# Optimization experiments

Measured on AMD Instinct MI355X. Metric: run time of the kernel, lower is better.

The kernel has to match this reference:

```python
import jax, jax.numpy as jnp
import numpy as np

N, HID, L, NC = 2048, 256, 4, 10
D0, D1, D2 = HID, HID // 2, HID // 8   # dims for degrees l=0,1,2
H, DH = 4, HID // 4                    # heads for degree-0 attention
F = D0 + D1 + D2                       # invariant feature width
C2 = float(np.sqrt(3.0))


def setup_inputs() -> dict:
    key = jax.random.key(0)
    ks = jax.random.split(key, 16)

    def w(k, shape, fan):
        return jax.random.normal(k, shape, jnp.float32) / np.float32(np.sqrt(fan))

    return {
        "x": jax.random.uniform(ks[0], (N, 118), jnp.float32),
        "pos": jax.random.normal(ks[1], (N, 3), jnp.float32) * 3.0,
        "emb_W": w(ks[2], (118, D0), 118),
        "emb_b": jnp.zeros((D0,), jnp.float32),
        "Wq": w(ks[3], (L, F, H * DH), F),
        "Wk": w(ks[4], (L, F, H * DH), F),
        "Wv0": w(ks[5], (L, D0, D0), D0),
        "Wv1": w(ks[6], (L, D1, D1), D1),
        "Wv2": w(ks[7], (L, D2, D2), D2),
        "Ws1": w(ks[8], (L, D0, D1), D0),
        "Ws2": w(ks[9], (L, D0, D2), D0),
        "Wffa": w(ks[10], (L, D0, 2 * D0), D0),
        "Wffb": w(ks[11], (L, 2 * D0, D0), 2 * D0),
        "Wg": w(ks[12], (L, F, D1 + D2), F),
        "out_W": w(ks[13], (D0, NC), D0),
        "out_b": jnp.zeros((NC,), jnp.float32),
    }


def _sph_harmonics(pos):
    """Real spherical harmonics Y1 [N,N,3], Y2 [N,N,5] of pairwise unit vectors."""
    rel = pos[None, :, :] - pos[:, None, :]                  # [N,N,3]
    dist = jnp.linalg.norm(rel, axis=-1, keepdims=True)
    valid = (dist > 1e-6).astype(pos.dtype)                  # zero out self-pairs
    u = rel / jnp.maximum(dist, 1e-6) * valid
    ux, uy, uz = u[..., 0], u[..., 1], u[..., 2]
    Y1 = u
    Y2 = jnp.stack([
        C2 * ux * uy,
        C2 * uy * uz,
        0.5 * (3.0 * uz * uz - 1.0),
        C2 * ux * uz,
        0.5 * C2 * (ux * ux - uy * uy),
    ], axis=-1) * valid                                      # [N,N,5]
    return Y1, Y2


def _invariants(x0, x1, x2):
    return jnp.concatenate([
        x0,
        jnp.linalg.norm(x1, axis=-1),
        jnp.linalg.norm(x2, axis=-1),
    ], axis=-1)                                              # [N,F]


def _layer(x0, x1, x2, Y1, Y2, Wq, Wk, Wv0, Wv1, Wv2, Ws1, Ws2, Wffa, Wffb, Wg):
    inv = _invariants(x0, x1, x2)
    q = (inv @ Wq).reshape(N, H, DH)
    k = (inv @ Wk).reshape(N, H, DH)
    attn = jax.nn.softmax(jnp.einsum('nhd,mhd->hnm', q, k) / np.float32(np.sqrt(DH)), axis=-1)

    # degree-0 aggregation (4 heads)
    v0 = (x0 @ Wv0).reshape(N, H, D0 // H)
    agg0 = jnp.einsum('hnm,mhc->nhc', attn, v0).reshape(N, D0)

    a = attn.mean(0)                                         # [N,N] single head for l>0
    # degree-1: channel-mixed values + degree-0 -> degree-1 via Y1
    v1 = jnp.einsum('mdc,de->mec', x1, Wv1)                  # [N,D1,3]
    agg1 = jnp.einsum('nm,mdc->ndc', a, v1)
    mix1 = jnp.einsum('nmc,md->ndc', a[:, :, None] * Y1, x0 @ Ws1)
    # degree-2: channel-mixed values + degree-0 -> degree-2 via Y2
    v2 = jnp.einsum('mdc,de->mec', x2, Wv2)                  # [N,D2,5]
    agg2 = jnp.einsum('nm,mdc->ndc', a, v2)
    mix2 = jnp.einsum('nmc,md->ndc', a[:, :, None] * Y2, x0 @ Ws2)

    x0 = x0 + agg0
    x1 = x1 + agg1 + mix1
    x2 = x2 + agg2 + mix2

    # gated equivariant feedforward
    x0 = x0 + jax.nn.silu(x0 @ Wffa) @ Wffb
    g = jax.nn.sigmoid(_invariants(x0, x1, x2) @ Wg)         # [N,D1+D2]
    x1 = x1 * g[:, :D1, None]
    x2 = x2 * g[:, D1:, None]
    return x0, x1, x2


def reference(x, pos, emb_W, emb_b, Wq, Wk, Wv0, Wv1, Wv2, Ws1, Ws2, Wffa, Wffb, Wg, out_W, out_b):
    Y1, Y2 = _sph_harmonics(pos)
    x0 = x @ emb_W + emb_b                                   # input embedding
    x1 = jnp.zeros((N, D1, 3), x0.dtype)
    x2 = jnp.zeros((N, D2, 5), x0.dtype)
    for l in range(L):
        x0, x1, x2 = _layer(x0, x1, x2, Y1, Y2,
                            Wq[l], Wk[l], Wv0[l], Wv1[l], Wv2[l],
                            Ws1[l], Ws2[l], Wffa[l], Wffb[l], Wg[l])
    return x0 @ out_W + out_b                                # [N, num_classes]
```

## Files before the change

kernel.cpp:

```cpp
#include <hip/hip_runtime.h>
#include <math.h>

#define N_    2048
#define D0_   256
#define D1_   128
#define D2_   32
#define F_    416
#define H_    4
#define DH_   64
#define L_    4
#define NC_   10
#define C2_   1.7320508075688772f
#define X12W  544

typedef unsigned short u16;
typedef __attribute__((ext_vector_type(8))) short short8v;
typedef __attribute__((ext_vector_type(4))) float f32x4;

union U8 { u16 u[8]; short8v v; };

__device__ __forceinline__ u16 f2bf(float f) {
    union { float f; unsigned int u; } x; x.f = f;
    unsigned int r = x.u + 0x7FFFu + ((x.u >> 16) & 1u);
    return (u16)(r >> 16);
}
__device__ __forceinline__ float bf2f(u16 u) {
    union { float f; unsigned int u; } x; x.u = ((unsigned int)u) << 16;
    return x.f;
}

__device__ __forceinline__ f32x4 mfma16(short8v a, short8v b, f32x4 c) {
    return __builtin_amdgcn_mfma_f32_16x16x32_bf16(a, b, c, 0, 0, 0);
}

enum { B_NN = 0, B_NT = 1 };
enum { EPI_STORE = 0, EPI_SILU = 1, EPI_SIGMOID = 2, EPI_ACCUM = 3, EPI_ATOMIC = 4,
       EPI_STOREB = 5 };

template<int BLAY, int EPI>
__global__ __launch_bounds__(256) void mfma_gemm(
    const float* __restrict__ A, int lda,
    const float* __restrict__ B, int ldb,
    const float* __restrict__ bias,
    float* __restrict__ C, int ldc,
    int M, int K, int Nn, float scale, int kchunk,
    int zk, long long Ah, long long Bh, long long Ch)
{
    __shared__ __align__(16) u16 As[64][40];
    __shared__ __align__(16) u16 Bs[64][40];
    const int t = threadIdx.x;
    const int bm = blockIdx.y * 64, bn = blockIdx.x * 64;
    const int hz = blockIdx.z / zk, kz = blockIdx.z % zk;
    A += (size_t)hz * Ah; B += (size_t)hz * Bh;
    const int lane = t & 63, w = t >> 6;
    const int r0 = (w >> 1) * 32, c0 = (w & 1) * 32;
    const int fr = lane & 15, fk = (lane >> 4) * 8;
    const int ml = t >> 2, k8 = (t & 3) * 8;
    const int kbeg = kz * kchunk;
    const int kend = (kbeg + kchunk < K) ? kbeg + kchunk : K;
    f32x4 acc[2][2] = {};

    for (int k0 = kbeg; k0 < kend; k0 += 32) {
        {
            U8 u;
            if (((lda & 3) == 0) && (k0 + 32 <= kend)) {
                const float* ap = A + (size_t)(bm + ml) * lda + k0 + k8;
                float4 a0 = *(const float4*)ap;
                float4 a1 = *(const float4*)(ap + 4);
                u.u[0]=f2bf(a0.x); u.u[1]=f2bf(a0.y); u.u[2]=f2bf(a0.z); u.u[3]=f2bf(a0.w);
                u.u[4]=f2bf(a1.x); u.u[5]=f2bf(a1.y); u.u[6]=f2bf(a1.z); u.u[7]=f2bf(a1.w);
            } else {
#pragma unroll
                for (int j = 0; j < 8; ++j) {
                    int kk = k0 + k8 + j;
                    u.u[j] = f2bf(kk < kend ? A[(size_t)(bm + ml) * lda + kk] : 0.f);
                }
            }
            *(short8v*)&As[ml][k8] = u.v;
        }
        {
            U8 u;
            if (BLAY == B_NT) {
                if (((ldb & 3) == 0) && (k0 + 32 <= kend) && (bn + ml < Nn)) {
                    const float* bp = B + (size_t)(bn + ml) * ldb + k0 + k8;
                    float4 b0 = *(const float4*)bp;
                    float4 b1 = *(const float4*)(bp + 4);
                    u.u[0]=f2bf(b0.x); u.u[1]=f2bf(b0.y); u.u[2]=f2bf(b0.z); u.u[3]=f2bf(b0.w);
                    u.u[4]=f2bf(b1.x); u.u[5]=f2bf(b1.y); u.u[6]=f2bf(b1.z); u.u[7]=f2bf(b1.w);
                } else {
#pragma unroll
                    for (int j = 0; j < 8; ++j) {
                        int kk = k0 + k8 + j;
                        u.u[j] = f2bf((kk < kend && bn + ml < Nn)
                                      ? B[(size_t)(bn + ml) * ldb + kk] : 0.f);
                    }
                }
            } else {
                int nc = bn + ml;
#pragma unroll
                for (int j = 0; j < 8; ++j) {
                    int kk = k0 + k8 + j;
                    u.u[j] = f2bf((kk < kend && nc < Nn) ? B[(size_t)kk * ldb + nc] : 0.f);
                }
            }
            *(short8v*)&Bs[ml][k8] = u.v;
        }
        __syncthreads();
        short8v a0 = *(const short8v*)&As[r0 + fr][fk];
        short8v a1 = *(const short8v*)&As[r0 + 16 + fr][fk];
        short8v b0 = *(const short8v*)&Bs[c0 + fr][fk];
        short8v b1 = *(const short8v*)&Bs[c0 + 16 + fr][fk];
        acc[0][0] = mfma16(a0, b0, acc[0][0]);
        acc[0][1] = mfma16(a0, b1, acc[0][1]);
        acc[1][0] = mfma16(a1, b0, acc[1][0]);
        acc[1][1] = mfma16(a1, b1, acc[1][1]);
        __syncthreads();
    }
#pragma unroll
    for (int mi = 0; mi < 2; ++mi)
#pragma unroll
    for (int ni = 0; ni < 2; ++ni)
#pragma unroll
    for (int r = 0; r < 4; ++r) {
        int row = bm + r0 + mi * 16 + ((lane >> 4) << 2) + r;
        int col = bn + c0 + ni * 16 + fr;
        if (col >= Nn) continue;
        float v = acc[mi][ni][r];
        if (EPI == EPI_STOREB) {
            ((u16*)C + (size_t)hz * Ch)[(size_t)row * ldc + col] = f2bf(v * scale);
        } else {
            float* cp = C + (size_t)hz * Ch + (size_t)row * ldc + col;
            if (EPI == EPI_STORE)   *cp = v * scale + (bias ? bias[col] : 0.f);
            if (EPI == EPI_SILU)    *cp = v / (1.f + expf(-v));
            if (EPI == EPI_SIGMOID) *cp = 1.f / (1.f + expf(-v));
            if (EPI == EPI_ACCUM)   *cp += v;
            if (EPI == EPI_ATOMIC)  atomicAdd(cp, v);
        }
    }
}

__global__ __launch_bounds__(256) void transpose_bf16(
    const float* __restrict__ in, u16* __restrict__ outT, int R, int C)
{
    __shared__ float tile[64][65];
    const int br = blockIdx.y * 64, bc = blockIdx.x * 64;
    const int t = threadIdx.x, lc = t & 63, q = t >> 6;
#pragma unroll 4
    for (int r = 0; r < 16; ++r) {
        int row = br + q * 16 + r, col = bc + lc;
        tile[q * 16 + r][lc] = (col < C) ? in[(size_t)row * C + col] : 0.f;
    }
    __syncthreads();
#pragma unroll 4
    for (int r = 0; r < 16; ++r) {
        int orow = bc + q * 16 + r;
        int ocol = br + lc;
        if (orow < C) outT[(size_t)orow * R + ocol] = f2bf(tile[lc][q * 16 + r]);
    }
}

template<int NB>
__global__ __launch_bounds__(256) void aggP(
    const u16* __restrict__ A, int lda,
    const u16* __restrict__ BT, int ldk,
    float* __restrict__ C, int ldc,
    int K, int Nn, int kchunk,
    int zk, long long Ah, long long Bh, long long Ch)
{
    __shared__ __align__(16) u16 As[64][40];
    __shared__ __align__(16) u16 Bs[NB][64][40];
    const int t = threadIdx.x;
    const int bm = blockIdx.y * 64, bn0 = blockIdx.x * 64 * NB;
    const int hz = blockIdx.z / zk, kz = blockIdx.z % zk;
    A += (size_t)hz * Ah; BT += (size_t)hz * Bh; C += (size_t)hz * Ch;
    const int lane = t & 63, w = t >> 6;
    const int r0 = (w >> 1) * 32, c0 = (w & 1) * 32;
    const int fr = lane & 15, fk = (lane >> 4) * 8;
    const int ml = t >> 2, k8 = (t & 3) * 8;
    const int kbeg = kz * kchunk;
    const int kend = (kbeg + kchunk < K) ? kbeg + kchunk : K;
    f32x4 acc[NB][2][2] = {};

    for (int k0 = kbeg; k0 < kend; k0 += 32) {
        *(short8v*)&As[ml][k8] = *(const short8v*)(A + (size_t)(bm + ml) * lda + k0 + k8);
#pragma unroll
        for (int nb = 0; nb < NB; ++nb) {
            int nc = bn0 + nb * 64 + ml;
            short8v z = {};
            *(short8v*)&Bs[nb][ml][k8] = (nc < Nn)
                ? *(const short8v*)(BT + (size_t)nc * ldk + k0 + k8) : z;
        }
        __syncthreads();
        short8v a0 = *(const short8v*)&As[r0 + fr][fk];
        short8v a1 = *(const short8v*)&As[r0 + 16 + fr][fk];
#pragma unroll
        for (int nb = 0; nb < NB; ++nb) {
            short8v b0 = *(const short8v*)&Bs[nb][c0 + fr][fk];
            short8v b1 = *(const short8v*)&Bs[nb][c0 + 16 + fr][fk];
            acc[nb][0][0] = mfma16(a0, b0, acc[nb][0][0]);
            acc[nb][0][1] = mfma16(a0, b1, acc[nb][0][1]);
            acc[nb][1][0] = mfma16(a1, b0, acc[nb][1][0]);
            acc[nb][1][1] = mfma16(a1, b1, acc[nb][1][1]);
        }
        __syncthreads();
    }
#pragma unroll
    for (int nb = 0; nb < NB; ++nb)
#pragma unroll
    for (int mi = 0; mi < 2; ++mi)
#pragma unroll
    for (int ni = 0; ni < 2; ++ni)
#pragma unroll
    for (int r = 0; r < 4; ++r) {
        int row = bm + r0 + mi * 16 + ((lane >> 4) << 2) + r;
        int col = bn0 + nb * 64 + c0 + ni * 16 + fr;
        if (col >= Nn) continue;
        atomicAdd(C + (size_t)row * ldc + col, acc[nb][mi][ni][r]);
    }
}

__global__ void ucompute_kernel(const float* __restrict__ pos, u16* __restrict__ U) {
    int idx = blockIdx.x * 256 + threadIdx.x;
    int n = idx >> 11, m = idx & (N_ - 1);
    float rx = pos[m * 3 + 0] - pos[n * 3 + 0];
    float ry = pos[m * 3 + 1] - pos[n * 3 + 1];
    float rz = pos[m * 3 + 2] - pos[n * 3 + 2];
    float d2 = rx * rx + ry * ry + rz * rz;
    bool valid = d2 > 1e-12f;
    float rinv = valid ? rsqrtf(d2) : 0.f;
    size_t base = (size_t)n * N_ + m;
    const size_t CS = (size_t)N_ * N_;
    U[base]          = f2bf(rx * rinv);
    U[base + CS]     = f2bf(ry * rinv);
    U[base + 2 * CS] = f2bf(rz * rinv);
}

__global__ __launch_bounds__(256) void mixc_kernel(
    const u16* __restrict__ amb, const u16* __restrict__ U,
    const u16* __restrict__ s1T, const u16* __restrict__ s2T,
    float* __restrict__ Macc)
{
    const int ch = blockIdx.z;
    const int gx = blockIdx.x;
    const bool deg1 = ch < 3;
    if (!deg1 && gx >= 8) return;
    const int bm = blockIdx.y * 64;
    const size_t CS = (size_t)N_ * N_;
    const int colbase = deg1 ? (gx & 1) * 64 : 0;
    const int ks      = deg1 ? (gx >> 1) : gx;
    const u16* BT     = deg1 ? s1T : s2T;
    __shared__ __align__(16) u16 As[64][40];
    __shared__ __align__(16) u16 Bs[64][40];
    const int t = threadIdx.x, lane = t & 63, w = t >> 6;
    const int r0 = (w >> 1) * 32, c0 = (w & 1) * 32;
    const int fr = lane & 15, fk = (lane >> 4) * 8;
    const int ml = t >> 2, k8 = (t & 3) * 8;
    const int kbeg = ks * 256, kend = kbeg + 256;
    f32x4 acc[2][2] = {};

    for (int m0 = kbeg; m0 < kend; m0 += 32) {
        const size_t off = (size_t)(bm + ml) * N_ + m0 + k8;
        U8 am8; am8.v = *(const short8v*)(amb + off);
        U8 o;
        if (deg1) {
            U8 uv; uv.v = *(const short8v*)(U + (size_t)ch * CS + off);
#pragma unroll
            for (int j = 0; j < 8; ++j)
                o.u[j] = f2bf(bf2f(am8.u[j]) * bf2f(uv.u[j]));
        } else {
            U8 xv, yv, zv;
            xv.v = *(const short8v*)(U + off);
            yv.v = *(const short8v*)(U + CS + off);
            zv.v = *(const short8v*)(U + 2 * CS + off);
#pragma unroll
            for (int j = 0; j < 8; ++j) {
                float a = bf2f(am8.u[j]);
                float ux = bf2f(xv.u[j]), uy = bf2f(yv.u[j]), uz = bf2f(zv.u[j]);
                float y;
                if      (ch == 3) y = C2_ * ux * uy;
                else if (ch == 4) y = C2_ * uy * uz;
                else if (ch == 5) y = (ux*ux + uy*uy + uz*uz > 0.5f)
                                      ? 0.5f * (3.f * uz * uz - 1.f) : 0.f;
                else if (ch == 6) y = C2_ * ux * uz;
                else              y = 0.5f * C2_ * (ux * ux - uy * uy);
                o.u[j] = f2bf(a * y);
            }
        }
        *(short8v*)&As[ml][k8] = o.v;
        {
            int nc = colbase + ml;
            short8v z = {};
            *(short8v*)&Bs[ml][k8] = (deg1 || nc < 32)
                ? *(const short8v*)(BT + (size_t)nc * N_ + m0 + k8) : z;
        }
        __syncthreads();
        short8v a0 = *(const short8v*)&As[r0 + fr][fk];
        short8v a1 = *(const short8v*)&As[r0 + 16 + fr][fk];
        short8v b0 = *(const short8v*)&Bs[c0 + fr][fk];
        short8v b1 = *(const short8v*)&Bs[c0 + 16 + fr][fk];
        acc[0][0] = mfma16(a0, b0, acc[0][0]);
        acc[0][1] = mfma16(a0, b1, acc[0][1]);
        acc[1][0] = mfma16(a1, b0, acc[1][0]);
        acc[1][1] = mfma16(a1, b1, acc[1][1]);
        __syncthreads();
    }
#pragma unroll
    for (int mi = 0; mi < 2; ++mi)
#pragma unroll
    for (int ni = 0; ni < 2; ++ni)
#pragma unroll
    for (int r = 0; r < 4; ++r) {
        int row = bm + r0 + mi * 16 + ((lane >> 4) << 2) + r;
        int col = colbase + c0 + ni * 16 + fr;
        float v = acc[mi][ni][r];
        if (deg1)
            atomicAdd(&Macc[(size_t)ch * N_ * 128 + (size_t)row * 128 + col], v);
        else if (col < 32)
            atomicAdd(&Macc[(size_t)3 * N_ * 128 + (size_t)(ch - 3) * N_ * 32
                            + (size_t)row * 32 + col], v);
    }
}

__global__ void mix_combine(const float* __restrict__ Macc, float* __restrict__ x12) {
    int idx = blockIdx.x * 256 + threadIdx.x;
    if (idx >= N_ * X12W) return;
    int n = idx / X12W, j = idx % X12W;
    float v;
    if (j < 384) {
        int e = j / 3, c = j - 3 * e;
        v = Macc[(size_t)c * N_ * 128 + (size_t)n * 128 + e];
    } else {
        int jj = j - 384;
        int e = jj / 5, c = jj - 5 * e;
        v = Macc[(size_t)3 * N_ * 128 + (size_t)c * N_ * 32 + (size_t)n * 32 + e];
    }
    x12[idx] += v;
}

__global__ void invar_kernel(const float* __restrict__ x0, const float* __restrict__ x12,
                             float* __restrict__ inv) {
    int n = blockIdx.x, t = threadIdx.x;
    inv[(size_t)n * F_ + t] = x0[(size_t)n * D0_ + t];
    if (t < 128) {
        const float* p = x12 + (size_t)n * X12W + t * 3;
        inv[(size_t)n * F_ + 256 + t] = sqrtf(p[0]*p[0] + p[1]*p[1] + p[2]*p[2]);
    }
    if (t < 32) {
        const float* p = x12 + (size_t)n * X12W + 384 + t * 5;
        inv[(size_t)n * F_ + 384 + t] =
            sqrtf(p[0]*p[0] + p[1]*p[1] + p[2]*p[2] + p[3]*p[3] + p[4]*p[4]);
    }
}

__global__ void v1_kernel(const float* __restrict__ x12, const float* __restrict__ W,
                          float* __restrict__ Vflat) {
    int m = blockIdx.x, t = threadIdx.x;
    __shared__ float sh[384];
    sh[t] = x12[(size_t)m * X12W + t];
    __syncthreads();
    int e = t / 3, c = t % 3;
    float acc = 0.f;
#pragma unroll 4
    for (int d = 0; d < 128; ++d)
        acc = fmaf(sh[d * 3 + c], W[d * 128 + e], acc);
    Vflat[(size_t)m * X12W + t] = acc;
}

__global__ void v2_kernel(const float* __restrict__ x12, const float* __restrict__ W,
                          float* __restrict__ Vflat) {
    int m = blockIdx.x, t = threadIdx.x;
    __shared__ float sh[160];
    if (t < 160) sh[t] = x12[(size_t)m * X12W + 384 + t];
    __syncthreads();
    if (t < 160) {
        int e = t / 5, c = t % 5;
        float acc = 0.f;
#pragma unroll 4
        for (int d = 0; d < 32; ++d)
            acc = fmaf(sh[d * 5 + c], W[d * 32 + e], acc);
        Vflat[(size_t)m * X12W + 384 + t] = acc;
    }
}

__global__ void softmax4(u16* __restrict__ Sb, u16* __restrict__ amb) {
    int n = blockIdx.x, t = threadIdx.x;
    __shared__ float red[256];
    const size_t NN = (size_t)N_ * N_;
    float amv[8] = {};
    for (int h = 0; h < H_; ++h) {
        u16* Sp = Sb + (size_t)h * NN + (size_t)n * N_ + t * 8;
        U8 sv; sv.v = *(const short8v*)Sp;
        float s[8];
#pragma unroll
        for (int j = 0; j < 8; ++j) s[j] = bf2f(sv.u[j]);
        float mx = s[0];
#pragma unroll
        for (int j = 1; j < 8; ++j) mx = fmaxf(mx, s[j]);
        red[t] = mx; __syncthreads();
        for (int st = 128; st > 0; st >>= 1) { if (t < st) red[t] = fmaxf(red[t], red[t + st]); __syncthreads(); }
        mx = red[0]; __syncthreads();
        float sum = 0.f;
#pragma unroll
        for (int j = 0; j < 8; ++j) { s[j] = expf(s[j] - mx); sum += s[j]; }
        red[t] = sum; __syncthreads();
        for (int st = 128; st > 0; st >>= 1) { if (t < st) red[t] += red[t + st]; __syncthreads(); }
        float rinv = 1.f / red[0]; __syncthreads();
        U8 pv;
#pragma unroll
        for (int j = 0; j < 8; ++j) {
            float p = s[j] * rinv;
            pv.u[j] = f2bf(p);
            amv[j] += 0.25f * p;
        }
        *(short8v*)Sp = pv.v;
    }
    U8 av;
#pragma unroll
    for (int j = 0; j < 8; ++j) av.u[j] = f2bf(amv[j]);
    *(short8v*)(amb + (size_t)n * N_ + t * 8) = av.v;
}

__global__ void gate_kernel(const float* __restrict__ g, float* __restrict__ x12) {
    int idx = blockIdx.x * 256 + threadIdx.x;
    if (idx >= N_ * X12W) return;
    int n = idx / X12W, j = idx % X12W;
    float gv = (j < 384) ? g[n * 160 + j / 3] : g[n * 160 + 128 + (j - 384) / 5];
    x12[idx] *= gv;
}

extern "C" void kernel_launch(void* const* d_in, const int* in_sizes, int n_in,
                              void* d_out, int out_size, void* d_ws, size_t ws_size,
                              hipStream_t stream) {
    const float* x    = (const float*)d_in[0];
    const float* pos  = (const float*)d_in[1];
    const float* embW = (const float*)d_in[2];
    const float* embB = (const float*)d_in[3];
    const float* Wq   = (const float*)d_in[4];
    const float* Wk   = (const float*)d_in[5];
    const float* Wv0  = (const float*)d_in[6];
    const float* Wv1  = (const float*)d_in[7];
    const float* Wv2  = (const float*)d_in[8];
    const float* Ws1  = (const float*)d_in[9];
    const float* Ws2  = (const float*)d_in[10];
    const float* Wffa = (const float*)d_in[11];
    const float* Wffb = (const float*)d_in[12];
    const float* Wg   = (const float*)d_in[13];
    const float* outW = (const float*)d_in[14];
    const float* outB = (const float*)d_in[15];
    float* out = (float*)d_out;

    const size_t NN = (size_t)N_ * N_;
    float* p = (float*)d_ws;
    float* x0    = p; p += N_ * D0_;
    float* x12   = p; p += N_ * X12W;
    float* inv   = p; p += N_ * F_;
    float* q     = p; p += N_ * D0_;
    float* k     = p; p += N_ * D0_;
    float* v0    = p; p += N_ * D0_;
    float* Vflat = p; p += N_ * X12W;
    float* s1    = p; p += N_ * D1_;
    float* s2    = p; p += N_ * D2_;
    float* fft   = p; p += N_ * 512;
    float* gm    = p; p += N_ * 160;
    float* Macc  = p; p += 3 * N_ * 128 + 5 * N_ * 32;
    u16* ub   = (u16*)p;
    u16* Sb   = ub; ub += 4 * NN;
    u16* amb  = ub; ub += NN;
    u16* U    = ub; ub += 3 * NN;
    u16* v0T  = ub; ub += D0_ * N_;
    u16* s1T  = ub; ub += D1_ * N_;
    u16* s2T  = ub; ub += D2_ * N_;
    u16* VflatT = ub; ub += X12W * N_;

    hipMemsetAsync(x12, 0, (size_t)N_ * X12W * sizeof(float), stream);
    ucompute_kernel<<<(N_ * N_) / 256, 256, 0, stream>>>(pos, U);

    mfma_gemm<B_NN, EPI_STORE><<<dim3(4, 32), 256, 0, stream>>>(
        x, 118, embW, 256, embB, x0, 256, N_, 118, 256, 1.f, 118, 1, 0, 0, 0);

    for (int l = 0; l < L_; ++l) {
        const float* Wq_l   = Wq   + (size_t)l * F_ * 256;
        const float* Wk_l   = Wk   + (size_t)l * F_ * 256;
        const float* Wv0_l  = Wv0  + (size_t)l * 256 * 256;
        const float* Wv1_l  = Wv1  + (size_t)l * 128 * 128;
        const float* Wv2_l  = Wv2  + (size_t)l * 32 * 32;
        const float* Ws1_l  = Ws1  + (size_t)l * 256 * 128;
        const float* Ws2_l  = Ws2  + (size_t)l * 256 * 32;
        const float* Wffa_l = Wffa + (size_t)l * 256 * 512;
        const float* Wffb_l = Wffb + (size_t)l * 512 * 256;
        const float* Wg_l   = Wg   + (size_t)l * F_ * 160;

        hipMemsetAsync(Macc, 0, (3 * N_ * 128 + 5 * N_ * 32) * sizeof(float), stream);
        invar_kernel<<<N_, 256, 0, stream>>>(x0, x12, inv);
        mfma_gemm<B_NN, EPI_STORE><<<dim3(4, 32), 256, 0, stream>>>(
            inv, F_, Wq_l, 256, nullptr, q, 256, N_, F_, 256, 1.f, F_, 1, 0, 0, 0);
        mfma_gemm<B_NN, EPI_STORE><<<dim3(4, 32), 256, 0, stream>>>(
            inv, F_, Wk_l, 256, nullptr, k, 256, N_, F_, 256, 1.f, F_, 1, 0, 0, 0);
        mfma_gemm<B_NN, EPI_STORE><<<dim3(4, 32), 256, 0, stream>>>(
            x0, 256, Wv0_l, 256, nullptr, v0, 256, N_, 256, 256, 1.f, 256, 1, 0, 0, 0);
        mfma_gemm<B_NN, EPI_STORE><<<dim3(2, 32), 256, 0, stream>>>(
            x0, 256, Ws1_l, 128, nullptr, s1, 128, N_, 256, 128, 1.f, 256, 1, 0, 0, 0);
        mfma_gemm<B_NN, EPI_STORE><<<dim3(1, 32), 256, 0, stream>>>(
            x0, 256, Ws2_l, 32, nullptr, s2, 32, N_, 256, 32, 1.f, 256, 1, 0, 0, 0);
        v1_kernel<<<N_, 384, 0, stream>>>(x12, Wv1_l, Vflat);
        v2_kernel<<<N_, 192, 0, stream>>>(x12, Wv2_l, Vflat);

        transpose_bf16<<<dim3(4, 32), 256, 0, stream>>>(v0, v0T, N_, 256);
        transpose_bf16<<<dim3(2, 32), 256, 0, stream>>>(s1, s1T, N_, 128);
        transpose_bf16<<<dim3(1, 32), 256, 0, stream>>>(s2, s2T, N_, 32);
        transpose_bf16<<<dim3(9, 32), 256, 0, stream>>>(Vflat, VflatT, N_, X12W);

        mfma_gemm<B_NT, EPI_STOREB><<<dim3(32, 32, 4), 256, 0, stream>>>(
            q, 256, k, 256, nullptr, (float*)Sb, N_, N_, 64, N_, 0.125f, 64,
            1, 64, 64, (long long)NN);
        softmax4<<<N_, 256, 0, stream>>>(Sb, amb);
        aggP<1><<<dim3(1, 32, 32), 256, 0, stream>>>(
            Sb, N_, v0T, N_, x0, 256, N_, 64, 256,
            8, (long long)NN, (long long)(64 * N_), 64);

        aggP<3><<<dim3(3, 32, 4), 256, 0, stream>>>(
            amb, N_, VflatT, N_, x12, X12W, N_, X12W, 512,
            4, 0, 0, 0);
        mixc_kernel<<<dim3(16, 32, 8), 256, 0, stream>>>(amb, U, s1T, s2T, Macc);
        mix_combine<<<(N_ * X12W + 255) / 256, 256, 0, stream>>>(Macc, x12);

        mfma_gemm<B_NN, EPI_SILU><<<dim3(8, 32), 256, 0, stream>>>(
            x0, 256, Wffa_l, 512, nullptr, fft, 512, N_, 256, 512, 1.f, 256, 1, 0, 0, 0);
        mfma_gemm<B_NN, EPI_ACCUM><<<dim3(4, 32), 256, 0, stream>>>(
            fft, 512, Wffb_l, 256, nullptr, x0, 256, N_, 512, 256, 1.f, 512, 1, 0, 0, 0);

        invar_kernel<<<N_, 256, 0, stream>>>(x0, x12, inv);
        mfma_gemm<B_NN, EPI_SIGMOID><<<dim3(3, 32), 256, 0, stream>>>(
            inv, F_, Wg_l, 160, nullptr, gm, 160, N_, F_, 160, 1.f, F_, 1, 0, 0, 0);
        gate_kernel<<<(N_ * X12W + 255) / 256, 256, 0, stream>>>(gm, x12);
    }

    mfma_gemm<B_NN, EPI_STORE><<<dim3(1, 32), 256, 0, stream>>>(
        x0, 256, outW, NC_, outB, out, NC_, N_, 256, NC_, 1.f, 256, 1, 0, 0, 0);
}
```

Before: 1.484 ms.

## Fuse attention into two-pass flash-style kernels and batch mix channels per block

Replaces the materialized 4-head bf16 score matrix, separate softmax and P·V aggregation with two kernels. The first computes per-row softmax max and normalizer online. The second recomputes scores, writes the head-averaged attention and accumulates P·V into x0 atomically. The mix kernel is split into degree-templated variants that reuse one loaded U/amb tile across all 3 or 5 channels instead of reloading it per channel. This removes large N×N×4 memory traffic, but the QK^T product is now computed twice and the pass-2 grid is small (128 blocks), which risks low occupancy.

```diff
diff --git a/kernel.cpp b/kernel.cpp
--- a/kernel.cpp
+++ b/kernel.cpp
@@ -28,14 +28,12 @@
     union { float f; unsigned int u; } x; x.u = ((unsigned int)u) << 16;
     return x.f;
 }
-
 __device__ __forceinline__ f32x4 mfma16(short8v a, short8v b, f32x4 c) {
     return __builtin_amdgcn_mfma_f32_16x16x32_bf16(a, b, c, 0, 0, 0);
 }
 
 enum { B_NN = 0, B_NT = 1 };
-enum { EPI_STORE = 0, EPI_SILU = 1, EPI_SIGMOID = 2, EPI_ACCUM = 3, EPI_ATOMIC = 4,
-       EPI_STOREB = 5 };
+enum { EPI_STORE = 0, EPI_SILU = 1, EPI_SIGMOID = 2, EPI_ACCUM = 3, EPI_ATOMIC = 4 };
 
 template<int BLAY, int EPI>
 __global__ __launch_bounds__(256) void mfma_gemm(
@@ -43,20 +41,17 @@
     const float* __restrict__ B, int ldb,
     const float* __restrict__ bias,
     float* __restrict__ C, int ldc,
-    int M, int K, int Nn, float scale, int kchunk,
-    int zk, long long Ah, long long Bh, long long Ch)
+    int M, int K, int Nn, float scale, int kchunk)
 {
     __shared__ __align__(16) u16 As[64][40];
     __shared__ __align__(16) u16 Bs[64][40];
     const int t = threadIdx.x;
     const int bm = blockIdx.y * 64, bn = blockIdx.x * 64;
-    const int hz = blockIdx.z / zk, kz = blockIdx.z % zk;
-    A += (size_t)hz * Ah; B += (size_t)hz * Bh;
     const int lane = t & 63, w = t >> 6;
     const int r0 = (w >> 1) * 32, c0 = (w & 1) * 32;
     const int fr = lane & 15, fk = (lane >> 4) * 8;
     const int ml = t >> 2, k8 = (t & 3) * 8;
-    const int kbeg = kz * kchunk;
+    const int kbeg = blockIdx.z * kchunk;
     const int kend = (kbeg + kchunk < K) ? kbeg + kchunk : K;
     f32x4 acc[2][2] = {};
 
@@ -81,19 +76,11 @@
         {
             U8 u;
             if (BLAY == B_NT) {
-                if (((ldb & 3) == 0) && (k0 + 32 <= kend) && (bn + ml < Nn)) {
-                    const float* bp = B + (size_t)(bn + ml) * ldb + k0 + k8;
-                    float4 b0 = *(const float4*)bp;
-                    float4 b1 = *(const float4*)(bp + 4);
-                    u.u[0]=f2bf(b0.x); u.u[1]=f2bf(b0.y); u.u[2]=f2bf(b0.z); u.u[3]=f2bf(b0.w);
-                    u.u[4]=f2bf(b1.x); u.u[5]=f2bf(b1.y); u.u[6]=f2bf(b1.z); u.u[7]=f2bf(b1.w);
-                } else {
-#pragma unroll
-                    for (int j = 0; j < 8; ++j) {
-                        int kk = k0 + k8 + j;
-                        u.u[j] = f2bf((kk < kend && bn + ml < Nn)
-                                      ? B[(size_t)(bn + ml) * ldb + kk] : 0.f);
-                    }
+#pragma unroll
+                for (int j = 0; j < 8; ++j) {
+                    int kk = k0 + k8 + j;
+                    u.u[j] = f2bf((kk < kend && bn + ml < Nn)
+                                  ? B[(size_t)(bn + ml) * ldb + kk] : 0.f);
                 }
             } else {
                 int nc = bn + ml;
@@ -126,16 +113,12 @@
         int col = bn + c0 + ni * 16 + fr;
         if (col >= Nn) continue;
         float v = acc[mi][ni][r];
-        if (EPI == EPI_STOREB) {
-            ((u16*)C + (size_t)hz * Ch)[(size_t)row * ldc + col] = f2bf(v * scale);
-        } else {
-            float* cp = C + (size_t)hz * Ch + (size_t)row * ldc + col;
-            if (EPI == EPI_STORE)   *cp = v * scale + (bias ? bias[col] : 0.f);
-            if (EPI == EPI_SILU)    *cp = v / (1.f + expf(-v));
-            if (EPI == EPI_SIGMOID) *cp = 1.f / (1.f + expf(-v));
-            if (EPI == EPI_ACCUM)   *cp += v;
-            if (EPI == EPI_ATOMIC)  atomicAdd(cp, v);
-        }
+        float* cp = C + (size_t)row * ldc + col;
+        if (EPI == EPI_STORE)   *cp = v * scale + (bias ? bias[col] : 0.f);
+        if (EPI == EPI_SILU)    *cp = v / (1.f + expf(-v));
+        if (EPI == EPI_SIGMOID) *cp = 1.f / (1.f + expf(-v));
+        if (EPI == EPI_ACCUM)   *cp += v;
+        if (EPI == EPI_ATOMIC)  atomicAdd(cp, v);
     }
 }
 
@@ -164,15 +147,13 @@
     const u16* __restrict__ A, int lda,
     const u16* __restrict__ BT, int ldk,
     float* __restrict__ C, int ldc,
-    int K, int Nn, int kchunk,
-    int zk, long long Ah, long long Bh, long long Ch)
+    int K, int Nn, int kchunk, int zk)
 {
     __shared__ __align__(16) u16 As[64][40];
     __shared__ __align__(16) u16 Bs[NB][64][40];
     const int t = threadIdx.x;
     const int bm = blockIdx.y * 64, bn0 = blockIdx.x * 64 * NB;
-    const int hz = blockIdx.z / zk, kz = blockIdx.z % zk;
-    A += (size_t)hz * Ah; BT += (size_t)hz * Bh; C += (size_t)hz * Ch;
+    const int kz = blockIdx.z % zk;
     const int lane = t & 63, w = t >> 6;
     const int r0 = (w >> 1) * 32, c0 = (w & 1) * 32;
     const int fr = lane & 15, fk = (lane >> 4) * 8;
@@ -235,75 +216,87 @@
     U[base + 2 * CS] = f2bf(rz * rinv);
 }
 
-__global__ __launch_bounds__(256) void mixc_kernel(
+template<int DEG>
+__global__ __launch_bounds__(256) void mixf_kernel(
     const u16* __restrict__ amb, const u16* __restrict__ U,
-    const u16* __restrict__ s1T, const u16* __restrict__ s2T,
-    float* __restrict__ Macc)
+    const u16* __restrict__ BT, float* __restrict__ Macc)
 {
-    const int ch = blockIdx.z;
-    const int gx = blockIdx.x;
-    const bool deg1 = ch < 3;
-    if (!deg1 && gx >= 8) return;
+    constexpr int NCH = (DEG == 1) ? 3 : 5;
+    constexpr int NCT = (DEG == 1) ? 2 : 1;
     const int bm = blockIdx.y * 64;
     const size_t CS = (size_t)N_ * N_;
-    const int colbase = deg1 ? (gx & 1) * 64 : 0;
-    const int ks      = deg1 ? (gx >> 1) : gx;
-    const u16* BT     = deg1 ? s1T : s2T;
-    __shared__ __align__(16) u16 As[64][40];
-    __shared__ __align__(16) u16 Bs[64][40];
+    __shared__ __align__(16) u16 As[NCH][64][40];
+    __shared__ __align__(16) u16 Bs[NCT][64][40];
     const int t = threadIdx.x, lane = t & 63, w = t >> 6;
     const int r0 = (w >> 1) * 32, c0 = (w & 1) * 32;
     const int fr = lane & 15, fk = (lane >> 4) * 8;
     const int ml = t >> 2, k8 = (t & 3) * 8;
-    const int kbeg = ks * 256, kend = kbeg + 256;
-    f32x4 acc[2][2] = {};
+    const int kbeg = blockIdx.x * 256, kend = kbeg + 256;
+    f32x4 acc[NCH][NCT][2][2] = {};
 
     for (int m0 = kbeg; m0 < kend; m0 += 32) {
         const size_t off = (size_t)(bm + ml) * N_ + m0 + k8;
         U8 am8; am8.v = *(const short8v*)(amb + off);
-        U8 o;
-        if (deg1) {
-            U8 uv; uv.v = *(const short8v*)(U + (size_t)ch * CS + off);
-#pragma unroll
-            for (int j = 0; j < 8; ++j)
-                o.u[j] = f2bf(bf2f(am8.u[j]) * bf2f(uv.u[j]));
+        U8 xv, yv, zv;
+        xv.v = *(const short8v*)(U + off);
+        yv.v = *(const short8v*)(U + CS + off);
+        zv.v = *(const short8v*)(U + 2 * CS + off);
+        if (DEG == 1) {
+            U8 o0, o1, o2;
+#pragma unroll
+            for (int j = 0; j < 8; ++j) {
+                float a = bf2f(am8.u[j]);
+                o0.u[j] = f2bf(a * bf2f(xv.u[j]));
+                o1.u[j] = f2bf(a * bf2f(yv.u[j]));
+                o2.u[j] = f2bf(a * bf2f(zv.u[j]));
+            }
+            *(short8v*)&As[0][ml][k8] = o0.v;
+            *(short8v*)&As[1][ml][k8] = o1.v;
+            *(short8v*)&As[2][ml][k8] = o2.v;
         } else {
-            U8 xv, yv, zv;
-            xv.v = *(const short8v*)(U + off);
-            yv.v = *(const short8v*)(U + CS + off);
-            zv.v = *(const short8v*)(U + 2 * CS + off);
+            U8 o[5];
 #pragma unroll
             for (int j = 0; j < 8; ++j) {
                 float a = bf2f(am8.u[j]);
                 float ux = bf2f(xv.u[j]), uy = bf2f(yv.u[j]), uz = bf2f(zv.u[j]);
-                float y;
-                if      (ch == 3) y = C2_ * ux * uy;
-                else if (ch == 4) y = C2_ * uy * uz;
-                else if (ch == 5) y = (ux*ux + uy*uy + uz*uz > 0.5f)
-                                      ? 0.5f * (3.f * uz * uz - 1.f) : 0.f;
-                else if (ch == 6) y = C2_ * ux * uz;
-                else              y = 0.5f * C2_ * (ux * ux - uy * uy);
-                o.u[j] = f2bf(a * y);
-            }
-        }
-        *(short8v*)&As[ml][k8] = o.v;
-        {
-            int nc = colbase + ml;
+                o[0].u[j] = f2bf(a * C2_ * ux * uy);
+                o[1].u[j] = f2bf(a * C2_ * uy * uz);
+                o[2].u[j] = f2bf((ux*ux + uy*uy + uz*uz > 0.5f)
+                                 ? a * 0.5f * (3.f * uz * uz - 1.f) : 0.f);
+                o[3].u[j] = f2bf(a * C2_ * ux * uz);
+                o[4].u[j] = f2bf(a * 0.5f * C2_ * (ux * ux - uy * uy));
+            }
+#pragma unroll
+            for (int c = 0; c < 5; ++c) *(short8v*)&As[c][ml][k8] = o[c].v;
+        }
+#pragma unroll
+        for (int ct = 0; ct < NCT; ++ct) {
+            int nc = ct * 64 + ml;
             short8v z = {};
-            *(short8v*)&Bs[ml][k8] = (deg1 || nc < 32)
+            *(short8v*)&Bs[ct][ml][k8] = (DEG == 1 || nc < 32)
                 ? *(const short8v*)(BT + (size_t)nc * N_ + m0 + k8) : z;
         }
         __syncthreads();
-        short8v a0 = *(const short8v*)&As[r0 + fr][fk];
-        short8v a1 = *(const short8v*)&As[r0 + 16 + fr][fk];
-        short8v b0 = *(const short8v*)&Bs[c0 + fr][fk];
-        short8v b1 = *(const short8v*)&Bs[c0 + 16 + fr][fk];
-        acc[0][0] = mfma16(a0, b0, acc[0][0]);
-        acc[0][1] = mfma16(a0, b1, acc[0][1]);
-        acc[1][0] = mfma16(a1, b0, acc[1][0]);
-        acc[1][1] = mfma16(a1, b1, acc[1][1]);
-        __syncthreads();
-    }
+#pragma unroll
+        for (int c = 0; c < NCH; ++c) {
+            short8v a0 = *(const short8v*)&As[c][r0 + fr][fk];
+            short8v a1 = *(const short8v*)&As[c][r0 + 16 + fr][fk];
+#pragma unroll
+            for (int ct = 0; ct < NCT; ++ct) {
+                short8v b0 = *(const short8v*)&Bs[ct][c0 + fr][fk];
+                short8v b1 = *(const short8v*)&Bs[ct][c0 + 16 + fr][fk];
+                acc[c][ct][0][0] = mfma16(a0, b0, acc[c][ct][0][0]);
+                acc[c][ct][0][1] = mfma16(a0, b1, acc[c][ct][0][1]);
+                acc[c][ct][1][0] = mfma16(a1, b0, acc[c][ct][1][0]);
+                acc[c][ct][1][1] = mfma16(a1, b1, acc[c][ct][1][1]);
+            }
+        }
+        __syncthreads();
+    }
+#pragma unroll
+    for (int c = 0; c < NCH; ++c)
+#pragma unroll
+    for (int ct = 0; ct < NCT; ++ct)
 #pragma unroll
     for (int mi = 0; mi < 2; ++mi)
 #pragma unroll
@@ -311,12 +304,12 @@
 #pragma unroll
     for (int r = 0; r < 4; ++r) {
         int row = bm + r0 + mi * 16 + ((lane >> 4) << 2) + r;
-        int col = colbase + c0 + ni * 16 + fr;
-        float v = acc[mi][ni][r];
-        if (deg1)
-            atomicAdd(&Macc[(size_t)ch * N_ * 128 + (size_t)row * 128 + col], v);
+        int col = ct * 64 + c0 + ni * 16 + fr;
+        float v = acc[c][ct][mi][ni][r];
+        if (DEG == 1)
+            atomicAdd(&Macc[(size_t)c * N_ * 128 + (size_t)row * 128 + col], v);
         else if (col < 32)
-            atomicAdd(&Macc[(size_t)3 * N_ * 128 + (size_t)(ch - 3) * N_ * 32
+            atomicAdd(&Macc[(size_t)3 * N_ * 128 + (size_t)c * N_ * 32
                             + (size_t)row * 32 + col], v);
     }
 }
@@ -335,6 +328,177 @@
         v = Macc[(size_t)3 * N_ * 128 + (size_t)c * N_ * 32 + (size_t)n * 32 + e];
     }
     x12[idx] += v;
+}
+
+__global__ __launch_bounds__(256) void attn_pass1(
+    const float* __restrict__ q, const float* __restrict__ k,
+    float* __restrict__ rsm, float* __restrict__ rsl)
+{
+    const int n0 = blockIdx.x * 64, h = blockIdx.y;
+    __shared__ __align__(16) u16 qs[64][72];
+    __shared__ __align__(16) u16 kt[64][72];
+    const int t = threadIdx.x, lane = t & 63, w = t >> 6;
+    const int fr = lane & 15, fk = (lane >> 4) * 8;
+    const int sr = t >> 2, sc = (t & 3) * 16;
+    {
+        const float* qp = q + (size_t)(n0 + sr) * 256 + h * 64 + sc;
+        U8 u0, u1;
+#pragma unroll
+        for (int j = 0; j < 8; ++j) { u0.u[j] = f2bf(qp[j]); u1.u[j] = f2bf(qp[8 + j]); }
+        *(short8v*)&qs[sr][sc] = u0.v;
+        *(short8v*)&qs[sr][sc + 8] = u1.v;
+    }
+    float mrun[4] = {-1e30f, -1e30f, -1e30f, -1e30f};
+    float lrun[4] = {};
+    const int rw = w * 16;
+
+    for (int m0 = 0; m0 < N_; m0 += 64) {
+        __syncthreads();
+        {
+            const float* kp = k + (size_t)(m0 + sr) * 256 + h * 64 + sc;
+            U8 u0, u1;
+#pragma unroll
+            for (int j = 0; j < 8; ++j) { u0.u[j] = f2bf(kp[j]); u1.u[j] = f2bf(kp[8 + j]); }
+            *(short8v*)&kt[sr][sc] = u0.v;
+            *(short8v*)&kt[sr][sc + 8] = u1.v;
+        }
+        __syncthreads();
+        short8v a0 = *(const short8v*)&qs[rw + fr][fk];
+        short8v a1 = *(const short8v*)&qs[rw + fr][32 + fk];
+        f32x4 sacc[4] = {};
+#pragma unroll
+        for (int ni = 0; ni < 4; ++ni) {
+            short8v b0 = *(const short8v*)&kt[ni * 16 + fr][fk];
+            short8v b1 = *(const short8v*)&kt[ni * 16 + fr][32 + fk];
+            sacc[ni] = mfma16(a1, b1, mfma16(a0, b0, sacc[ni]));
+        }
+#pragma unroll
+        for (int r = 0; r < 4; ++r) {
+            float tm = -1e30f;
+#pragma unroll
+            for (int ni = 0; ni < 4; ++ni) tm = fmaxf(tm, sacc[ni][r] * 0.125f);
+            tm = fmaxf(tm, __shfl_xor(tm, 1));
+            tm = fmaxf(tm, __shfl_xor(tm, 2));
+            tm = fmaxf(tm, __shfl_xor(tm, 4));
+            tm = fmaxf(tm, __shfl_xor(tm, 8));
+            float mn = fmaxf(mrun[r], tm);
+            float ts = 0.f;
+#pragma unroll
+            for (int ni = 0; ni < 4; ++ni) ts += expf(sacc[ni][r] * 0.125f - mn);
+            ts += __shfl_xor(ts, 1);
+            ts += __shfl_xor(ts, 2);
+            ts += __shfl_xor(ts, 4);
+            ts += __shfl_xor(ts, 8);
+            lrun[r] = lrun[r] * expf(mrun[r] - mn) + ts;
+            mrun[r] = mn;
+        }
+    }
+    if (fr == 0) {
+#pragma unroll
+        for (int r = 0; r < 4; ++r) {
+            int row = n0 + rw + (lane >> 4) * 4 + r;
+            rsm[(size_t)h * N_ + row] = mrun[r];
+            rsl[(size_t)h * N_ + row] = 1.f / lrun[r];
+        }
+    }
+}
+
+__global__ __launch_bounds__(256) void attn_pass2(
+    const float* __restrict__ q, const float* __restrict__ k,
+    const u16* __restrict__ v0T,
+    const float* __restrict__ rsm, const float* __restrict__ rsl,
+    u16* __restrict__ amb, float* __restrict__ x0)
+{
+    const int n0 = blockIdx.x * 64, mbase = blockIdx.y * 512;
+    __shared__ __align__(16) u16 qs[64][264];
+    __shared__ __align__(16) u16 kt[64][72];
+    __shared__ __align__(16) u16 vt[64][72];
+    __shared__ __align__(16) u16 Plds[4][16][72];
+    const int t = threadIdx.x, lane = t & 63, w = t >> 6;
+    const int fr = lane & 15, fk = (lane >> 4) * 8;
+    const int sr = t >> 2, sc = (t & 3) * 16;
+    const int rw = w * 16;
+    {
+#pragma unroll
+        for (int seg = 0; seg < 4; ++seg) {
+            const float* qp = q + (size_t)(n0 + sr) * 256 + seg * 64 + sc;
+            U8 u0, u1;
+#pragma unroll
+            for (int j = 0; j < 8; ++j) { u0.u[j] = f2bf(qp[j]); u1.u[j] = f2bf(qp[8 + j]); }
+            *(short8v*)&qs[sr][seg * 64 + sc] = u0.v;
+            *(short8v*)&qs[sr][seg * 64 + sc + 8] = u1.v;
+        }
+    }
+    f32x4 oacc[4][4] = {};
+
+    for (int mt = 0; mt < 8; ++mt) {
+        const int m0 = mbase + mt * 64;
+        f32x4 amac[4] = {};
+#pragma unroll
+        for (int h = 0; h < 4; ++h) {
+            __syncthreads();
+            {
+                const float* kp = k + (size_t)(m0 + sr) * 256 + h * 64 + sc;
+                U8 u0, u1;
+#pragma unroll
+                for (int j = 0; j < 8; ++j) { u0.u[j] = f2bf(kp[j]); u1.u[j] = f2bf(kp[8 + j]); }
+                *(short8v*)&kt[sr][sc] = u0.v;
+                *(short8v*)&kt[sr][sc + 8] = u1.v;
+                *(short8v*)&vt[sr][sc] =
+                    *(const short8v*)(v0T + (size_t)(h * 64 + sr) * N_ + m0 + sc);
+                *(short8v*)&vt[sr][sc + 8] =
+                    *(const short8v*)(v0T + (size_t)(h * 64 + sr) * N_ + m0 + sc + 8);
+            }
+            __syncthreads();
+            short8v a0 = *(const short8v*)&qs[rw + fr][h * 64 + fk];
+            short8v a1 = *(const short8v*)&qs[rw + fr][h * 64 + 32 + fk];
+            float mf[4], lf[4];
+#pragma unroll
+            for (int r = 0; r < 4; ++r) {
+                int row = n0 + rw + (lane >> 4) * 4 + r;
+                mf[r] = rsm[(size_t)h * N_ + row];
+                lf[r] = rsl[(size_t)h * N_ + row];
+            }
+#pragma unroll
+            for (int ni = 0; ni < 4; ++ni) {
+                short8v b0 = *(const short8v*)&kt[ni * 16 + fr][fk];
+                short8v b1 = *(const short8v*)&kt[ni * 16 + fr][32 + fk];
+                f32x4 sacc = {};
+                sacc = mfma16(a1, b1, mfma16(a0, b0, sacc));
+#pragma unroll
+                for (int r = 0; r < 4; ++r) {
+                    float pv = expf(sacc[r] * 0.125f - mf[r]) * lf[r];
+                    amac[ni][r] += 0.25f * pv;
+                    Plds[w][(lane >> 4) * 4 + r][ni * 16 + fr] = f2bf(pv);
+                }
+            }
+            __syncthreads();
+            short8v pa0 = *(const short8v*)&Plds[w][fr][fk];
+            short8v pa1 = *(const short8v*)&Plds[w][fr][32 + fk];
+#pragma unroll
+            for (int ni = 0; ni < 4; ++ni) {
+                short8v b0 = *(const short8v*)&vt[ni * 16 + fr][fk];
+                short8v b1 = *(const short8v*)&vt[ni * 16 + fr][32 + fk];
+                oacc[h][ni] = mfma16(pa1, b1, mfma16(pa0, b0, oacc[h][ni]));
+            }
+        }
+#pragma unroll
+        for (int ni = 0; ni < 4; ++ni)
+#pragma unroll
+        for (int r = 0; r < 4; ++r) {
+            int row = n0 + rw + (lane >> 4) * 4 + r;
+            amb[(size_t)row * N_ + m0 + ni * 16 + fr] = f2bf(amac[ni][r]);
+        }
+    }
+#pragma unroll
+    for (int h = 0; h < 4; ++h)
+#pragma unroll
+    for (int ni = 0; ni < 4; ++ni)
+#pragma unroll
+    for (int r = 0; r < 4; ++r) {
+        int row = n0 + rw + (lane >> 4) * 4 + r;
+        atomicAdd(&x0[(size_t)row * 256 + h * 64 + ni * 16 + fr], oacc[h][ni][r]);
+    }
 }
 
 __global__ void invar_kernel(const float* __restrict__ x0, const float* __restrict__ x12,
@@ -380,44 +544,6 @@
             acc = fmaf(sh[d * 5 + c], W[d * 32 + e], acc);
         Vflat[(size_t)m * X12W + 384 + t] = acc;
     }
-}
-
-__global__ void softmax4(u16* __restrict__ Sb, u16* __restrict__ amb) {
-    int n = blockIdx.x, t = threadIdx.x;
-    __shared__ float red[256];
-    const size_t NN = (size_t)N_ * N_;
-    float amv[8] = {};
-    for (int h = 0; h < H_; ++h) {
-        u16* Sp = Sb + (size_t)h * NN + (size_t)n * N_ + t * 8;
-        U8 sv; sv.v = *(const short8v*)Sp;
-        float s[8];
-#pragma unroll
-        for (int j = 0; j < 8; ++j) s[j] = bf2f(sv.u[j]);
-        float mx = s[0];
-#pragma unroll
-        for (int j = 1; j < 8; ++j) mx = fmaxf(mx, s[j]);
-        red[t] = mx; __syncthreads();
-        for (int st = 128; st > 0; st >>= 1) { if (t < st) red[t] = fmaxf(red[t], red[t + st]); __syncthreads(); }
-        mx = red[0]; __syncthreads();
-        float sum = 0.f;
-#pragma unroll
-        for (int j = 0; j < 8; ++j) { s[j] = expf(s[j] - mx); sum += s[j]; }
-        red[t] = sum; __syncthreads();
-        for (int st = 128; st > 0; st >>= 1) { if (t < st) red[t] += red[t + st]; __syncthreads(); }
-        float rinv = 1.f / red[0]; __syncthreads();
-        U8 pv;
-#pragma unroll
-        for (int j = 0; j < 8; ++j) {
-            float p = s[j] * rinv;
-            pv.u[j] = f2bf(p);
-            amv[j] += 0.25f * p;
-        }
-        *(short8v*)Sp = pv.v;
-    }
-    U8 av;
-#pragma unroll
-    for (int j = 0; j < 8; ++j) av.u[j] = f2bf(amv[j]);
-    *(short8v*)(amb + (size_t)n * N_ + t * 8) = av.v;
 }
 
 __global__ void gate_kernel(const float* __restrict__ g, float* __restrict__ x12) {
@@ -463,8 +589,9 @@
     float* fft   = p; p += N_ * 512;
     float* gm    = p; p += N_ * 160;
     float* Macc  = p; p += 3 * N_ * 128 + 5 * N_ * 32;
+    float* rsm   = p; p += H_ * N_;
+    float* rsl   = p; p += H_ * N_;
     u16* ub   = (u16*)p;
-    u16* Sb   = ub; ub += 4 * NN;
     u16* amb  = ub; ub += NN;
     u16* U    = ub; ub += 3 * NN;
     u16* v0T  = ub; ub += D0_ * N_;
@@ -476,7 +603,7 @@
     ucompute_kernel<<<(N_ * N_) / 256, 256, 0, stream>>>(pos, U);
 
     mfma_gemm<B_NN, EPI_STORE><<<dim3(4, 32), 256, 0, stream>>>(
-        x, 118, embW, 256, embB, x0, 256, N_, 118, 256, 1.f, 118, 1, 0, 0, 0);
+        x, 118, embW, 256, embB, x0, 256, N_, 118, 256, 1.f, 118);
 
     for (int l = 0; l < L_; ++l) {
         const float* Wq_l   = Wq   + (size_t)l * F_ * 256;
@@ -493,15 +620,15 @@
         hipMemsetAsync(Macc, 0, (3 * N_ * 128 + 5 * N_ * 32) * sizeof(float), stream);
         invar_kernel<<<N_, 256, 0, stream>>>(x0, x12, inv);
         mfma_gemm<B_NN, EPI_STORE><<<dim3(4, 32), 256, 0, stream>>>(
-            inv, F_, Wq_l, 256, nullptr, q, 256, N_, F_, 256, 1.f, F_, 1, 0, 0, 0);
+            inv, F_, Wq_l, 256, nullptr, q, 256, N_, F_, 256, 1.f, F_);
         mfma_gemm<B_NN, EPI_STORE><<<dim3(4, 32), 256, 0, stream>>>(
-            inv, F_, Wk_l, 256, nullptr, k, 256, N_, F_, 256, 1.f, F_, 1, 0, 0, 0);
+            inv, F_, Wk_l, 256, nullptr, k, 256, N_, F_, 256, 1.f, F_);
         mfma_gemm<B_NN, EPI_STORE><<<dim3(4, 32), 256, 0, stream>>>(
-            x0, 256, Wv0_l, 256, nullptr, v0, 256, N_, 256, 256, 1.f, 256, 1, 0, 0, 0);
+            x0, 256, Wv0_l, 256, nullptr, v0, 256, N_, 256, 256, 1.f, 256);
         mfma_gemm<B_NN, EPI_STORE><<<dim3(2, 32), 256, 0, stream>>>(
-            x0, 256, Ws1_l, 128, nullptr, s1, 128, N_, 256, 128, 1.f, 256, 1, 0, 0, 0);
+            x0, 256, Ws1_l, 128, nullptr, s1, 128, N_, 256, 128, 1.f, 256);
         mfma_gemm<B_NN, EPI_STORE><<<dim3(1, 32), 256, 0, stream>>>(
-            x0, 256, Ws2_l, 32, nullptr, s2, 32, N_, 256, 32, 1.f, 256, 1, 0, 0, 0);
+            x0, 256, Ws2_l, 32, nullptr, s2, 32, N_, 256, 32, 1.f, 256);
         v1_kernel<<<N_, 384, 0, stream>>>(x12, Wv1_l, Vflat);
         v2_kernel<<<N_, 192, 0, stream>>>(x12, Wv2_l, Vflat);
 
@@ -510,31 +637,26 @@
         transpose_bf16<<<dim3(1, 32), 256, 0, stream>>>(s2, s2T, N_, 32);
         transpose_bf16<<<dim3(9, 32), 256, 0, stream>>>(Vflat, VflatT, N_, X12W);
 
-        mfma_gemm<B_NT, EPI_STOREB><<<dim3(32, 32, 4), 256, 0, stream>>>(
-            q, 256, k, 256, nullptr, (float*)Sb, N_, N_, 64, N_, 0.125f, 64,
-            1, 64, 64, (long long)NN);
-        softmax4<<<N_, 256, 0, stream>>>(Sb, amb);
-        aggP<1><<<dim3(1, 32, 32), 256, 0, stream>>>(
-            Sb, N_, v0T, N_, x0, 256, N_, 64, 256,
-            8, (long long)NN, (long long)(64 * N_), 64);
+        attn_pass1<<<dim3(32, 4), 256, 0, stream>>>(q, k, rsm, rsl);
+        attn_pass2<<<dim3(32, 4), 256, 0, stream>>>(q, k, v0T, rsm, rsl, amb, x0);
 
         aggP<3><<<dim3(3, 32, 4), 256, 0, stream>>>(
-            amb, N_, VflatT, N_, x12, X12W, N_, X12W, 512,
-            4, 0, 0, 0);
-        mixc_kernel<<<dim3(16, 32, 8), 256, 0, stream>>>(amb, U, s1T, s2T, Macc);
+            amb, N_, VflatT, N_, x12, X12W, N_, X12W, 512, 4);
+        mixf_kernel<1><<<dim3(8, 32), 256, 0, stream>>>(amb, U, s1T, Macc);
+        mixf_kernel<2><<<dim3(8, 32), 256, 0, stream>>>(amb, U, s2T, Macc);
         mix_combine<<<(N_ * X12W + 255) / 256, 256, 0, stream>>>(Macc, x12);
 
         mfma_gemm<B_NN, EPI_SILU><<<dim3(8, 32), 256, 0, stream>>>(
-            x0, 256, Wffa_l, 512, nullptr, fft, 512, N_, 256, 512, 1.f, 256, 1, 0, 0, 0);
+            x0, 256, Wffa_l, 512, nullptr, fft, 512, N_, 256, 512, 1.f, 256);
         mfma_gemm<B_NN, EPI_ACCUM><<<dim3(4, 32), 256, 0, stream>>>(
-            fft, 512, Wffb_l, 256, nullptr, x0, 256, N_, 512, 256, 1.f, 512, 1, 0, 0, 0);
+            fft, 512, Wffb_l, 256, nullptr, x0, 256, N_, 512, 256, 1.f, 512);
 
         invar_kernel<<<N_, 256, 0, stream>>>(x0, x12, inv);
         mfma_gemm<B_NN, EPI_SIGMOID><<<dim3(3, 32), 256, 0, stream>>>(
-            inv, F_, Wg_l, 160, nullptr, gm, 160, N_, F_, 160, 1.f, F_, 1, 0, 0, 0);
+            inv, F_, Wg_l, 160, nullptr, gm, 160, N_, F_, 160, 1.f, F_);
         gate_kernel<<<(N_ * X12W + 255) / 256, 256, 0, stream>>>(gm, x12);
     }
 
     mfma_gemm<B_NN, EPI_STORE><<<dim3(1, 32), 256, 0, stream>>>(
-        x0, 256, outW, NC_, outB, out, NC_, N_, 256, NC_, 1.f, 256, 1, 0, 0, 0);
-}
+        x0, 256, outW, NC_, outB, out, NC_, N_, 256, NC_, 1.f, 256);
+}
```

After: 1.843 ms. +24.2%, slower.
